# Performance work log

Measured on AMD Instinct MI355X. Metric: run time of the kernel, lower is better.

Reference implementation:

```python
import jax, jax.numpy as jnp
import numpy as np

B, N, F, H, ITERS = 128, 512, 8, 128, 3


def setup_inputs() -> dict:
    key = jax.random.key(0)
    ks = jax.random.split(key, 20)
    s = lambda d: 1.0 / np.sqrt(d)
    inp = {
        "jets": jax.random.normal(ks[0], (B, N, F), dtype=jnp.float32),
        "mask": jnp.ones((B, N), dtype=jnp.float32),
        # embedding: 2-layer MLP (emb_init=2)
        "emb_W0": jax.random.normal(ks[1], (F, H), jnp.float32) * s(F),
        "emb_b0": jnp.zeros((H,), jnp.float32),
        "emb_W1": jax.random.normal(ks[2], (H, H), jnp.float32) * s(H),
        "emb_b1": jnp.zeros((H,), jnp.float32),
        # MP layers (stacked over iters): message MLP + vertex update MLP
        "mp_Wm": jax.random.normal(ks[3], (ITERS, H, H), jnp.float32) * s(H),
        "mp_bm": jnp.zeros((ITERS, H), jnp.float32),
        "mp_Wu": jax.random.normal(ks[4], (ITERS, 2 * H, H), jnp.float32) * s(2 * H),
        "mp_bu": jnp.zeros((ITERS, H), jnp.float32),
        # simple readout: sum-pool then 2-layer MLP
        "ro_W1": jax.random.normal(ks[5], (H, H), jnp.float32) * s(H),
        "ro_b1": jnp.zeros((H,), jnp.float32),
        "ro_W2": jax.random.normal(ks[6], (H, H), jnp.float32) * s(H),
        "ro_b2": jnp.zeros((H,), jnp.float32),
    }
    return inp


def _adjacency(jets, mask):
    # fixed Gaussian-kernel affinity on raw features, row-softmax normalized
    sq = jnp.sum(jets * jets, axis=-1)                      # [B,N]
    d2 = sq[:, :, None] + sq[:, None, :] - 2.0 * jnp.einsum("bif,bjf->bij", jets, jets)
    logits = -d2 + jnp.where(mask[:, None, :] > 0, 0.0, -1e9)  # mask columns
    return jax.nn.softmax(logits, axis=-1)                  # [B,N,N]


def reference(jets, mask, emb_W0, emb_b0, emb_W1, emb_b1,
              mp_Wm, mp_bm, mp_Wu, mp_bu, ro_W1, ro_b1, ro_W2, ro_b2):
    # embedding
    h = jax.nn.relu(jnp.einsum("bnf,fh->bnh", jets, emb_W0) + emb_b0)
    h = jax.nn.relu(jnp.einsum("bnh,hk->bnk", h, emb_W1) + emb_b1)
    dij = _adjacency(jets, mask)                            # fixed across iterations
    m3 = mask[:, :, None]
    for t in range(ITERS):  # small fixed iteration count
        msg = jax.nn.relu(jnp.einsum("bnh,hk->bnk", h, mp_Wm[t]) + mp_bm[t])
        agg = jnp.einsum("bij,bjh->bih", dij, msg)          # gather+aggregate over adjacency
        h = jax.nn.relu(jnp.einsum("bnh,hk->bnk", jnp.concatenate([h, agg], axis=-1), mp_Wu[t]) + mp_bu[t])
        h = h * m3
    pooled = jnp.sum(h * m3, axis=1)                        # [B,H]
    out = jax.nn.relu(pooled @ ro_W1 + ro_b1) @ ro_W2 + ro_b2
    return out
```

## Files before the change

### kernel.cpp

```cpp
#include <hip/hip_runtime.h>
#include <stdint.h>
#include <stddef.h>

#define Bb 128
#define Nn 512
#define Hh 128
#define ROWS (Bb*Nn)

typedef __bf16 bf16;
typedef __bf16 bf16x2 __attribute__((ext_vector_type(2)));
typedef __bf16 bf16x4 __attribute__((ext_vector_type(4)));
typedef __bf16 bf16x8 __attribute__((ext_vector_type(8)));
typedef float  f32x4  __attribute__((ext_vector_type(4)));

__device__ __forceinline__ void glds16(const void* g, void* l) {
  __builtin_amdgcn_global_load_lds(
      (const __attribute__((address_space(1))) void*)g,
      (__attribute__((address_space(3))) void*)l, 16, 0, 0);
}


__global__ __launch_bounds__(256) void prep_all(
    const float* __restrict__ eW1, const float* __restrict__ Wm,
    const float* __restrict__ Wu, bf16* __restrict__ WTe,
    bf16* __restrict__ WmF, bf16* __restrict__ WuF) {
  int idx = blockIdx.x*256 + threadIdx.x;
  if (idx < 16384) {
    int k = idx >> 7, c = idx & 127;
    WTe[c*128 + (k ^ ((c & 7) << 3))] = (bf16)eW1[idx];
  } else if (idx < 65536) {
    int sub = idx - 16384;
    int s = sub >> 14, r = sub & 16383;
    int k = r >> 7, c = r & 127;
    WmF[s*16384 + (((c>>4)*4 + (k>>5))*64 + ((k>>3)&3)*16 + (c&15))*8 + (k&7)] = (bf16)Wm[sub];
  } else if (idx < 65536 + 98304) {
    int sub = idx - 65536;
    int s = sub >> 15, r = sub & 32767;
    int k = r >> 7, c = r & 127;
    WuF[s*32768 + (((c>>4)*8 + (k>>5))*64 + ((k>>3)&3)*16 + (c&15))*8 + (k&7)] = (bf16)Wu[sub];
  }
}

__global__ __launch_bounds__(256) void pmat_kernel(
    const float* __restrict__ jets, const float* __restrict__ mask,
    bf16* __restrict__ PF, float* __restrict__ rsum) {
  __shared__ float Xs[Nn*9];
  __shared__ float cbs[Nn];
  const int t = threadIdx.x;
  const int b = blockIdx.x & 127, ic = blockIdx.x >> 7;
  const int i0 = ic*128;
  const float* jb = jets + (size_t)b*Nn*8;
  for (int j = t; j < Nn; j += 256) {
    float s2 = 0.f;
#pragma unroll
    for (int f = 0; f < 8; ++f) { float v = jb[j*8+f]; Xs[j*9+f] = v; s2 = fmaf(v,v,s2); }
    cbs[j] = s2 + (mask[(size_t)b*Nn+j] > 0.f ? 0.f : 1e9f);
  }
  __syncthreads();
  const int w = t >> 6, lane = t & 63, l15 = lane & 15, g = lane >> 4;
  const int i0w = i0 + w*32;
  float xi2[2][8], sqi[2], lsum[2];
#pragma unroll
  for (int r = 0; r < 2; ++r) {
    int i = i0w + r*16 + l15;
    float sq = 0.f;
#pragma unroll
    for (int f = 0; f < 8; ++f) {
      float v = Xs[i*9+f];
      xi2[r][f] = 2.f*v;
      sq = fmaf(v, v, sq);
    }
    sqi[r] = sq;
    lsum[r] = 0.f;
  }
  bf16* Pr[2];
#pragma unroll
  for (int r = 0; r < 2; ++r) {
    int it = (i0w >> 4) + r;
    Pr[r] = PF + (((size_t)b*32 + it)*16)*512 + lane*8;
  }
#pragma unroll 2
  for (int j0 = 0; j0 < Nn; j0 += 32) {
    bf16x8 pfr[2];
#pragma unroll
    for (int e = 0; e < 8; ++e) {
      int j = j0 + 8*g + e;
      float xj[8];
#pragma unroll
      for (int f = 0; f < 8; ++f) xj[f] = Xs[j*9+f];
      float cb = cbs[j];
      float d0 = -(cb + sqi[0]);
      float d1 = -(cb + sqi[1]);
#pragma unroll
      for (int f = 0; f < 8; ++f) {
        d0 = fmaf(xi2[0][f], xj[f], d0);
        d1 = fmaf(xi2[1][f], xj[f], d1);
      }
      float ev0 = __expf(d0), ev1 = __expf(d1);
      lsum[0] += ev0; lsum[1] += ev1;
      pfr[0][e] = (bf16)ev0;
      pfr[1][e] = (bf16)ev1;
    }
#pragma unroll
    for (int r = 0; r < 2; ++r)
      *(bf16x8*)(Pr[r] + (j0 >> 5)*512) = pfr[r];
  }
#pragma unroll
  for (int r = 0; r < 2; ++r) {
    float s = lsum[r];
    s += __shfl_xor(s, 16, 64);
    s += __shfl_xor(s, 32, 64);
    if (g == 0) rsum[(size_t)b*Nn + i0w + r*16 + l15] = 1.f/s;
  }
}

__global__ __launch_bounds__(256) void embed_msg0(
    const float* __restrict__ jets, const float* __restrict__ W0,
    const float* __restrict__ b0, const bf16* __restrict__ WTe,
    const float* __restrict__ b1, const bf16* __restrict__ WmF0,
    const float* __restrict__ bm0, bf16* __restrict__ h,
    bf16* __restrict__ msgF) {
  __shared__ float sW0[8*128];
  __shared__ float sb0[128];
  __shared__ bf16 h0s[128*128];
  __shared__ bf16 sWT[128*128];
  const int t = threadIdx.x;
  const int w = t >> 6, lane = t & 63, l15 = lane & 15, g = lane >> 4;
  const int row_blk = blockIdx.x*128;
  for (int q = w; q < 32; q += 4)
    glds16((const char*)WTe + q*1024 + lane*16, (char*)(void*)sWT + q*1024);
  for (int i = t; i < 8*128; i += 256) sW0[i] = W0[i];
  if (t < 128) sb0[t] = b0[t];
  __syncthreads();
  {
    const int row = t & 127, colbase = (t >> 7) * 64;
    const float4* jp = (const float4*)(jets + ((size_t)row_blk + row)*8);
    float4 x0 = jp[0], x1 = jp[1];
    float x[8] = {x0.x,x0.y,x0.z,x0.w,x1.x,x1.y,x1.z,x1.w};
    const int sw = (row & 7) << 3;
#pragma unroll
    for (int cg = 0; cg < 16; ++cg) {
      int c0 = colbase + cg*4;
      bf16x4 o;
#pragma unroll
      for (int j = 0; j < 4; ++j) {
        float a = sb0[c0+j];
#pragma unroll
        for (int f = 0; f < 8; ++f) a = fmaf(x[f], sW0[f*128 + c0 + j], a);
        o[j] = (bf16)fmaxf(a, 0.f);
      }
      *(bf16x4*)(h0s + row*128 + (c0 ^ sw)) = o;
    }
  }
  __syncthreads();
  const int wr = (w & 1)*64, wc = (w >> 1)*64;
  f32x4 acc[4][4];
#pragma unroll
  for (int m = 0; m < 4; ++m)
#pragma unroll
    for (int n = 0; n < 4; ++n) acc[m][n] = (f32x4){0.f,0.f,0.f,0.f};
#pragma unroll
  for (int kk = 0; kk < 128; kk += 32) {
    bf16x8 bfr[4], wfr[4];
#pragma unroll
    for (int n = 0; n < 4; ++n) {
      int row = wr + n*16 + l15;
      bfr[n] = *(const bf16x8*)(h0s + row*128 + ((kk + 8*g) ^ ((row & 7) << 3)));
    }
#pragma unroll
    for (int m = 0; m < 4; ++m) {
      int c = wc + m*16 + l15;
      wfr[m] = *(const bf16x8*)(sWT + c*128 + ((kk + 8*g) ^ ((c & 7) << 3)));
    }
#pragma unroll
    for (int m = 0; m < 4; ++m)
#pragma unroll
      for (int n = 0; n < 4; ++n)
        acc[m][n] = __builtin_amdgcn_mfma_f32_16x16x32_bf16(wfr[m], bfr[n], acc[m][n], 0,0,0);
  }
  __syncthreads();
#pragma unroll
  for (int m = 0; m < 4; ++m) {
    f32x4 bs = *(const f32x4*)(b1 + wc + m*16 + g*4);
#pragma unroll
    for (int n = 0; n < 4; ++n) {
      int lr = wr + n*16 + l15;
      int r = row_blk + lr;
      int c0 = wc + m*16 + g*4;
      bf16x4 o;
#pragma unroll
      for (int j = 0; j < 4; ++j) o[j] = (bf16)fmaxf(acc[m][n][j] + bs[j], 0.f);
      *(bf16x4*)(h + (size_t)r*128 + c0) = o;
      *(bf16x4*)(h0s + lr*128 + (c0 ^ ((lr & 7) << 3))) = o;
    }
  }
  __syncthreads();
  {
    f32x4 acc2[4][4];
#pragma unroll
    for (int m = 0; m < 4; ++m)
#pragma unroll
      for (int n = 0; n < 4; ++n) acc2[m][n] = (f32x4){0.f,0.f,0.f,0.f};
#pragma unroll
    for (int kk = 0; kk < 128; kk += 32) {
      bf16x8 bfr[4], wfr[4];
#pragma unroll
      for (int n = 0; n < 4; ++n) {
        int lr = wr + n*16 + l15;
        bfr[n] = *(const bf16x8*)(h0s + lr*128 + ((kk + 8*g) ^ ((lr & 7) << 3)));
      }
#pragma unroll
      for (int m = 0; m < 4; ++m) {
        int cblk = (wc >> 4) + m;
        wfr[m] = *(const bf16x8*)(WmF0 + (size_t)(cblk*4 + (kk >> 5))*512 + lane*8);
      }
#pragma unroll
      for (int m = 0; m < 4; ++m)
#pragma unroll
        for (int n = 0; n < 4; ++n)
          acc2[m][n] = __builtin_amdgcn_mfma_f32_16x16x32_bf16(bfr[n], wfr[m], acc2[m][n], 0,0,0);
    }
    const int b = row_blk >> 9;
    const int rbase = (row_blk & 511) + wr;
#pragma unroll
    for (int m = 0; m < 4; ++m) {
      int c = wc + m*16 + l15;
      int mblk = (wc >> 4) + m;
      float bc = bm0[c];
#pragma unroll
      for (int n = 0; n < 4; ++n) {
        int rl = rbase + n*16 + g*4;
        bf16x4 o;
#pragma unroll
        for (int j = 0; j < 4; ++j) o[j] = (bf16)fmaxf(acc2[m][n][j] + bc, 0.f);
        size_t off = (size_t)b*65536 + (size_t)((rl>>5)*8 + mblk)*512
                   + (((rl>>3)&3)*16 + l15)*8 + (rl&7);
        *(bf16x4*)(msgF + off) = o;
      }
    }
  }
}

template<bool DO_MSG>
__global__ __launch_bounds__(256, 1) void iter_fused(
    const bf16* __restrict__ PF, const float* __restrict__ rsum,
    const float* __restrict__ mask, const bf16* __restrict__ msgFin,
    bf16* __restrict__ h,
    const bf16* __restrict__ WuF, const float* __restrict__ bu,
    const bf16* __restrict__ WmF, const float* __restrict__ bm,
    bf16* __restrict__ msgFout) {
  __shared__ __align__(16) char smem[65536];
  bf16* htile = (bf16*)smem;
  bf16* aggs  = (bf16*)(smem + 32768);
  const int t = threadIdx.x;
  const int b  = blockIdx.x & 127;
  const int ic = blockIdx.x >> 7;
  const int i0 = ic*128;
  const int w = t >> 6, lane = t & 63, l15 = lane & 15, g = lane >> 4;

  {
    const int i0w = i0 + w*32;
    float r_i[2];
#pragma unroll
    for (int r = 0; r < 2; ++r) r_i[r] = rsum[(size_t)b*Nn + i0w + r*16 + l15];
    f32x4 acc[2][8];
#pragma unroll
    for (int r = 0; r < 2; ++r)
#pragma unroll
      for (int m = 0; m < 8; ++m) acc[r][m] = (f32x4){0.f,0.f,0.f,0.f};
    const bf16* mBF = msgFin + (size_t)b*65536 + lane*8;
    const bf16* pBF = PF + ((size_t)b*32 + (i0w >> 4))*16*512 + lane*8;

    bf16x8 afrA[8], afrB[8], pfrA[2], pfrB[2];
    auto loadA = [&](int kt) {
#pragma unroll
      for (int m = 0; m < 8; ++m) afrA[m] = *(const bf16x8*)(mBF + (kt*8 + m)*512);
      pfrA[0] = *(const bf16x8*)(pBF + kt*512);
      pfrA[1] = *(const bf16x8*)(pBF + (16 + kt)*512);
    };
    auto loadB = [&](int kt) {
#pragma unroll
      for (int m = 0; m < 8; ++m) afrB[m] = *(const bf16x8*)(mBF + (kt*8 + m)*512);
      pfrB[0] = *(const bf16x8*)(pBF + kt*512);
      pfrB[1] = *(const bf16x8*)(pBF + (16 + kt)*512);
    };
    auto compute = [&](const bf16x8* afr, const bf16x8* pfr) {
#pragma unroll
      for (int m = 0; m < 8; ++m) {
        acc[0][m] = __builtin_amdgcn_mfma_f32_16x16x32_bf16(afr[m], pfr[0], acc[0][m], 0,0,0);
        acc[1][m] = __builtin_amdgcn_mfma_f32_16x16x32_bf16(afr[m], pfr[1], acc[1][m], 0,0,0);
      }
    };

    loadA(0);
#pragma unroll
    for (int kt = 0; kt < 16; kt += 2) {
      loadB(kt + 1);
      compute(afrA, pfrA);
      if (kt + 2 < 16) loadA(kt + 2);
      compute(afrB, pfrB);
    }
#pragma unroll
    for (int r = 0; r < 2; ++r) {
      int lr = w*32 + r*16 + l15;
#pragma unroll
      for (int m = 0; m < 8; ++m) {
        bf16x4 o;
#pragma unroll
        for (int j = 0; j < 4; ++j) o[j] = (bf16)(acc[r][m][j] * r_i[r]);
        int c0 = m*16 + g*4;
        *(bf16x4*)(aggs + lr*128 + (c0 ^ ((lr & 7) << 3))) = o;
      }
    }
  }
  __syncthreads();

  const int wr = (w & 1)*64, wc = (w >> 1)*64;
  const size_t growbase = (size_t)b*Nn + i0;
  {
    f32x4 acc[4][4];
#pragma unroll
    for (int m = 0; m < 4; ++m)
#pragma unroll
      for (int n = 0; n < 4; ++n) acc[m][n] = (f32x4){0.f,0.f,0.f,0.f};
#pragma unroll
    for (int kk = 0; kk < 256; kk += 32) {
      bf16x8 bfr[4];
      if (kk < 128) {
#pragma unroll
        for (int n = 0; n < 4; ++n)
          bfr[n] = *(const bf16x8*)(h + (growbase + wr + n*16 + l15)*128 + kk + 8*g);
      } else {
#pragma unroll
        for (int n = 0; n < 4; ++n) {
          int lr = wr + n*16 + l15;
          int kl = (kk - 128) + 8*g;
          bfr[n] = *(const bf16x8*)(aggs + lr*128 + (kl ^ ((lr & 7) << 3)));
        }
      }
      bf16x8 wfr[4];
#pragma unroll
      for (int m = 0; m < 4; ++m) {
        int cblk = (wc >> 4) + m;
        wfr[m] = *(const bf16x8*)(WuF + (size_t)(cblk*8 + (kk >> 5))*512 + lane*8);
      }
#pragma unroll
      for (int m = 0; m < 4; ++m)
#pragma unroll
        for (int n = 0; n < 4; ++n)
          acc[m][n] = __builtin_amdgcn_mfma_f32_16x16x32_bf16(wfr[m], bfr[n], acc[m][n], 0,0,0);
    }
    __syncthreads();
#pragma unroll
    for (int m = 0; m < 4; ++m) {
      f32x4 bs = *(const f32x4*)(bu + wc + m*16 + g*4);
#pragma unroll
      for (int n = 0; n < 4; ++n) {
        int lr = wr + n*16 + l15;
        size_t r = growbase + lr;
        float mv = mask[r];
        bf16x4 o;
#pragma unroll
        for (int j = 0; j < 4; ++j)
          o[j] = (bf16)(fmaxf(acc[m][n][j] + bs[j], 0.f) * mv);
        int c0 = wc + m*16 + g*4;
        *(bf16x4*)(h + r*128 + c0) = o;
        if (DO_MSG)
          *(bf16x4*)(htile + lr*128 + (c0 ^ ((lr & 7) << 3))) = o;
      }
    }
  }
  if (!DO_MSG) return;
  __syncthreads();

  {
    f32x4 acc[4][4];
#pragma unroll
    for (int m = 0; m < 4; ++m)
#pragma unroll
      for (int n = 0; n < 4; ++n) acc[m][n] = (f32x4){0.f,0.f,0.f,0.f};
#pragma unroll
    for (int kk = 0; kk < 128; kk += 32) {
      bf16x8 bfr[4], wfr[4];
#pragma unroll
      for (int n = 0; n < 4; ++n) {
        int lr = wr + n*16 + l15;
        bfr[n] = *(const bf16x8*)(htile + lr*128 + ((kk + 8*g) ^ ((lr & 7) << 3)));
      }
#pragma unroll
      for (int m = 0; m < 4; ++m) {
        int cblk = (wc >> 4) + m;
        wfr[m] = *(const bf16x8*)(WmF + (size_t)(cblk*4 + (kk >> 5))*512 + lane*8);
      }
#pragma unroll
      for (int m = 0; m < 4; ++m)
#pragma unroll
        for (int n = 0; n < 4; ++n)
          acc[m][n] = __builtin_amdgcn_mfma_f32_16x16x32_bf16(bfr[n], wfr[m], acc[m][n], 0,0,0);
    }
#pragma unroll
    for (int m = 0; m < 4; ++m) {
      int c = wc + m*16 + l15;
      int mblk = (wc >> 4) + m;
      float bc = bm[c];
#pragma unroll
      for (int n = 0; n < 4; ++n) {
        int rl = i0 + wr + n*16 + g*4;
        bf16x4 o;
#pragma unroll
        for (int j = 0; j < 4; ++j) o[j] = (bf16)fmaxf(acc[m][n][j] + bc, 0.f);
        size_t off = (size_t)b*65536 + (size_t)((rl>>5)*8 + mblk)*512
                   + (((rl>>3)&3)*16 + l15)*8 + (rl&7);
        *(bf16x4*)(msgFout + off) = o;
      }
    }
  }
}

__global__ __launch_bounds__(256) void pool_readout(
    const bf16* __restrict__ h, const float* __restrict__ mask,
    const float* __restrict__ W1, const float* __restrict__ b1,
    const float* __restrict__ W2, const float* __restrict__ b2,
    float* __restrict__ out) {
  __shared__ float part[3][128];
  __shared__ float pl[128];
  __shared__ float hid[128];
  int b = blockIdx.x, t = threadIdx.x, g = t >> 6, cp = (t & 63)*2;
  float a0 = 0.f, a1 = 0.f;
  for (int n = g*128; n < g*128+128; ++n) {
    float mv = mask[(size_t)b*Nn + n];
    bf16x2 v = *(const bf16x2*)(h + ((size_t)b*Nn + n)*128 + cp);
    a0 = fmaf((float)v[0], mv, a0);
    a1 = fmaf((float)v[1], mv, a1);
  }
  if (g > 0) { part[g-1][cp] = a0; part[g-1][cp+1] = a1; }
  __syncthreads();
  if (g == 0) {
    pl[cp]   = a0 + part[0][cp]   + part[1][cp]   + part[2][cp];
    pl[cp+1] = a1 + part[0][cp+1] + part[1][cp+1] + part[2][cp+1];
  }
  __syncthreads();
  if (t < 128) {
    float a = b1[t];
#pragma unroll 4
    for (int j = 0; j < 128; ++j) a = fmaf(pl[j], W1[j*128 + t], a);
    hid[t] = fmaxf(a, 0.f);
  }
  __syncthreads();
  if (t < 128) {
    float a = b2[t];
#pragma unroll 4
    for (int j = 0; j < 128; ++j) a = fmaf(hid[j], W2[j*128 + t], a);
    out[(size_t)b*128 + t] = a;
  }
}

extern "C" void kernel_launch(void* const* d_in, const int* in_sizes, int n_in,
                              void* d_out, int out_size, void* d_ws, size_t ws_size,
                              hipStream_t stream) {
  const float* jets = (const float*)d_in[0];
  const float* mask = (const float*)d_in[1];
  const float* eW0  = (const float*)d_in[2];
  const float* eb0  = (const float*)d_in[3];
  const float* eW1  = (const float*)d_in[4];
  const float* eb1  = (const float*)d_in[5];
  const float* Wm   = (const float*)d_in[6];
  const float* bm   = (const float*)d_in[7];
  const float* Wu   = (const float*)d_in[8];
  const float* bu   = (const float*)d_in[9];
  const float* rW1  = (const float*)d_in[10];
  const float* rb1  = (const float*)d_in[11];
  const float* rW2  = (const float*)d_in[12];
  const float* rb2  = (const float*)d_in[13];
  float* out = (float*)d_out;

  bf16* h     = (bf16*)d_ws;
  bf16* msgFA = h     + (size_t)ROWS*128;
  bf16* msgFB = msgFA + (size_t)ROWS*128;
  bf16* PF    = msgFB + (size_t)ROWS*128;
  bf16* WTe   = PF    + (size_t)Bb*512*512;
  bf16* WmF   = WTe   + 128*128;
  bf16* WuF   = WmF   + 3*128*128;
  float* rsum = (float*)(WuF + 3*256*128);

  prep_all<<<640, 256, 0, stream>>>(eW1, Wm, Wu, WTe, WmF, WuF);
  pmat_kernel<<<Bb*4, 256, 0, stream>>>(jets, mask, PF, rsum);
  embed_msg0<<<ROWS/128, 256, 0, stream>>>(jets, eW0, eb0, WTe, eb1,
                                           WmF, bm, h, msgFA);
  iter_fused<true><<<Bb*4, 256, 0, stream>>>(
      PF, rsum, mask, msgFA, h,
      WuF, bu, WmF + (size_t)1*128*128, bm + 1*128, msgFB);
  iter_fused<true><<<Bb*4, 256, 0, stream>>>(
      PF, rsum, mask, msgFB, h,
      WuF + (size_t)1*256*128, bu + 1*128,
      WmF + (size_t)2*128*128, bm + 2*128, msgFA);
  iter_fused<false><<<Bb*4, 256, 0, stream>>>(
      PF, rsum, mask, msgFA, h,
      WuF + (size_t)2*256*128, bu + 2*128, nullptr, nullptr, nullptr);

  pool_readout<<<Bb, 256, 0, stream>>>(h, mask, rW1, rb1, rW2, rb2, out);
}
```

Before: 158.5 us.

## Fuse adjacency matrix generation into first message-passing iteration kernel

Result: slower. 167.9 us (+5.9%).

```diff
diff --git a/kernel.cpp b/kernel.cpp
--- a/kernel.cpp
+++ b/kernel.cpp
@@ -41,79 +41,6 @@
   }
 }
 
-__global__ __launch_bounds__(256) void pmat_kernel(
-    const float* __restrict__ jets, const float* __restrict__ mask,
-    bf16* __restrict__ PF, float* __restrict__ rsum) {
-  __shared__ float Xs[Nn*9];
-  __shared__ float cbs[Nn];
-  const int t = threadIdx.x;
-  const int b = blockIdx.x & 127, ic = blockIdx.x >> 7;
-  const int i0 = ic*128;
-  const float* jb = jets + (size_t)b*Nn*8;
-  for (int j = t; j < Nn; j += 256) {
-    float s2 = 0.f;
-#pragma unroll
-    for (int f = 0; f < 8; ++f) { float v = jb[j*8+f]; Xs[j*9+f] = v; s2 = fmaf(v,v,s2); }
-    cbs[j] = s2 + (mask[(size_t)b*Nn+j] > 0.f ? 0.f : 1e9f);
-  }
-  __syncthreads();
-  const int w = t >> 6, lane = t & 63, l15 = lane & 15, g = lane >> 4;
-  const int i0w = i0 + w*32;
-  float xi2[2][8], sqi[2], lsum[2];
-#pragma unroll
-  for (int r = 0; r < 2; ++r) {
-    int i = i0w + r*16 + l15;
-    float sq = 0.f;
-#pragma unroll
-    for (int f = 0; f < 8; ++f) {
-      float v = Xs[i*9+f];
-      xi2[r][f] = 2.f*v;
-      sq = fmaf(v, v, sq);
-    }
-    sqi[r] = sq;
-    lsum[r] = 0.f;
-  }
-  bf16* Pr[2];
-#pragma unroll
-  for (int r = 0; r < 2; ++r) {
-    int it = (i0w >> 4) + r;
-    Pr[r] = PF + (((size_t)b*32 + it)*16)*512 + lane*8;
-  }
-#pragma unroll 2
-  for (int j0 = 0; j0 < Nn; j0 += 32) {
-    bf16x8 pfr[2];
-#pragma unroll
-    for (int e = 0; e < 8; ++e) {
-      int j = j0 + 8*g + e;
-      float xj[8];
-#pragma unroll
-      for (int f = 0; f < 8; ++f) xj[f] = Xs[j*9+f];
-      float cb = cbs[j];
-      float d0 = -(cb + sqi[0]);
-      float d1 = -(cb + sqi[1]);
-#pragma unroll
-      for (int f = 0; f < 8; ++f) {
-        d0 = fmaf(xi2[0][f], xj[f], d0);
-        d1 = fmaf(xi2[1][f], xj[f], d1);
-      }
-      float ev0 = __expf(d0), ev1 = __expf(d1);
-      lsum[0] += ev0; lsum[1] += ev1;
-      pfr[0][e] = (bf16)ev0;
-      pfr[1][e] = (bf16)ev1;
-    }
-#pragma unroll
-    for (int r = 0; r < 2; ++r)
-      *(bf16x8*)(Pr[r] + (j0 >> 5)*512) = pfr[r];
-  }
-#pragma unroll
-  for (int r = 0; r < 2; ++r) {
-    float s = lsum[r];
-    s += __shfl_xor(s, 16, 64);
-    s += __shfl_xor(s, 32, 64);
-    if (g == 0) rsum[(size_t)b*Nn + i0w + r*16 + l15] = 1.f/s;
-  }
-}
-
 __global__ __launch_bounds__(256) void embed_msg0(
     const float* __restrict__ jets, const float* __restrict__ W0,
     const float* __restrict__ b0, const bf16* __restrict__ WTe,
@@ -241,9 +168,10 @@
   }
 }
 
-template<bool DO_MSG>
+template<bool COMPUTE_P, bool DO_MSG>
 __global__ __launch_bounds__(256, 1) void iter_fused(
-    const bf16* __restrict__ PF, const float* __restrict__ rsum,
+    const float* __restrict__ jets, bf16* __restrict__ PF,
+    float* __restrict__ rsum,
     const float* __restrict__ mask, const bf16* __restrict__ msgFin,
     bf16* __restrict__ h,
     const bf16* __restrict__ WuF, const float* __restrict__ bu,
@@ -252,38 +180,95 @@
   __shared__ __align__(16) char smem[65536];
   bf16* htile = (bf16*)smem;
   bf16* aggs  = (bf16*)(smem + 32768);
+  float* Xs   = (float*)smem;
+  float* cbs  = (float*)(smem + 18432);
   const int t = threadIdx.x;
   const int b  = blockIdx.x & 127;
   const int ic = blockIdx.x >> 7;
   const int i0 = ic*128;
   const int w = t >> 6, lane = t & 63, l15 = lane & 15, g = lane >> 4;
 
+  if (COMPUTE_P) {
+    const float* jb = jets + (size_t)b*Nn*8;
+    for (int j = t; j < Nn; j += 256) {
+      float s2 = 0.f;
+#pragma unroll
+      for (int f = 0; f < 8; ++f) { float v = jb[j*8+f]; Xs[j*9+f] = v; s2 = fmaf(v,v,s2); }
+      cbs[j] = s2 + (mask[(size_t)b*Nn+j] > 0.f ? 0.f : 1e9f);
+    }
+    __syncthreads();
+  }
+
   {
     const int i0w = i0 + w*32;
-    float r_i[2];
-#pragma unroll
-    for (int r = 0; r < 2; ++r) r_i[r] = rsum[(size_t)b*Nn + i0w + r*16 + l15];
+    float r_i[2], lsum[2] = {0.f, 0.f};
+    float xi2[2][8], sqi[2];
+    if (COMPUTE_P) {
+#pragma unroll
+      for (int r = 0; r < 2; ++r) {
+        int i = i0w + r*16 + l15;
+        float sq = 0.f;
+#pragma unroll
+        for (int f = 0; f < 8; ++f) {
+          float v = Xs[i*9+f];
+          xi2[r][f] = 2.f*v;
+          sq = fmaf(v, v, sq);
+        }
+        sqi[r] = sq;
+      }
+    } else {
+#pragma unroll
+      for (int r = 0; r < 2; ++r) r_i[r] = rsum[(size_t)b*Nn + i0w + r*16 + l15];
+    }
     f32x4 acc[2][8];
 #pragma unroll
     for (int r = 0; r < 2; ++r)
 #pragma unroll
       for (int m = 0; m < 8; ++m) acc[r][m] = (f32x4){0.f,0.f,0.f,0.f};
     const bf16* mBF = msgFin + (size_t)b*65536 + lane*8;
-    const bf16* pBF = PF + ((size_t)b*32 + (i0w >> 4))*16*512 + lane*8;
+    bf16* pBF = PF + ((size_t)b*32 + (i0w >> 4))*16*512 + lane*8;
 
     bf16x8 afrA[8], afrB[8], pfrA[2], pfrB[2];
-    auto loadA = [&](int kt) {
+    auto loadAfrA = [&](int kt) {
 #pragma unroll
       for (int m = 0; m < 8; ++m) afrA[m] = *(const bf16x8*)(mBF + (kt*8 + m)*512);
+    };
+    auto loadAfrB = [&](int kt) {
+#pragma unroll
+      for (int m = 0; m < 8; ++m) afrB[m] = *(const bf16x8*)(mBF + (kt*8 + m)*512);
+    };
+    auto loadPfrA = [&](int kt) {
       pfrA[0] = *(const bf16x8*)(pBF + kt*512);
       pfrA[1] = *(const bf16x8*)(pBF + (16 + kt)*512);
     };
-    auto loadB = [&](int kt) {
-#pragma unroll
-      for (int m = 0; m < 8; ++m) afrB[m] = *(const bf16x8*)(mBF + (kt*8 + m)*512);
+    auto loadPfrB = [&](int kt) {
       pfrB[0] = *(const bf16x8*)(pBF + kt*512);
       pfrB[1] = *(const bf16x8*)(pBF + (16 + kt)*512);
     };
+    auto makeP = [&](int kt, bf16x8* pfr) {
+      int j0 = kt*32;
+#pragma unroll
+      for (int e = 0; e < 8; ++e) {
+        int j = j0 + 8*g + e;
+        float xj[8];
+#pragma unroll
+        for (int f = 0; f < 8; ++f) xj[f] = Xs[j*9+f];
+        float cb = cbs[j];
+        float d0 = -(cb + sqi[0]);
+        float d1 = -(cb + sqi[1]);
+#pragma unroll
+        for (int f = 0; f < 8; ++f) {
+          d0 = fmaf(xi2[0][f], xj[f], d0);
+          d1 = fmaf(xi2[1][f], xj[f], d1);
+        }
+        float ev0 = __expf(d0), ev1 = __expf(d1);
+        lsum[0] += ev0; lsum[1] += ev1;
+        pfr[0][e] = (bf16)ev0;
+        pfr[1][e] = (bf16)ev1;
+      }
+      *(bf16x8*)(pBF + kt*512)        = pfr[0];
+      *(bf16x8*)(pBF + (16 + kt)*512) = pfr[1];
+    };
     auto compute = [&](const bf16x8* afr, const bf16x8* pfr) {
 #pragma unroll
       for (int m = 0; m < 8; ++m) {
@@ -292,13 +277,27 @@
       }
     };
 
-    loadA(0);
+    loadAfrA(0);
+    if (!COMPUTE_P) loadPfrA(0);
 #pragma unroll
     for (int kt = 0; kt < 16; kt += 2) {
-      loadB(kt + 1);
+      loadAfrB(kt + 1);
+      if (COMPUTE_P) makeP(kt, pfrA); else loadPfrB(kt + 1);
       compute(afrA, pfrA);
-      if (kt + 2 < 16) loadA(kt + 2);
+      if (kt + 2 < 16) loadAfrA(kt + 2);
+      if (COMPUTE_P) makeP(kt + 1, pfrB);
+      else if (kt + 2 < 16) loadPfrA(kt + 2);
       compute(afrB, pfrB);
+    }
+    if (COMPUTE_P) {
+#pragma unroll
+      for (int r = 0; r < 2; ++r) {
+        float s = lsum[r];
+        s += __shfl_xor(s, 16, 64);
+        s += __shfl_xor(s, 32, 64);
+        r_i[r] = 1.f/s;
+        if (g == 0) rsum[(size_t)b*Nn + i0w + r*16 + l15] = r_i[r];
+      }
     }
 #pragma unroll
     for (int r = 0; r < 2; ++r) {
@@ -484,18 +483,17 @@
   float* rsum = (float*)(WuF + 3*256*128);
 
   prep_all<<<640, 256, 0, stream>>>(eW1, Wm, Wu, WTe, WmF, WuF);
-  pmat_kernel<<<Bb*4, 256, 0, stream>>>(jets, mask, PF, rsum);
   embed_msg0<<<ROWS/128, 256, 0, stream>>>(jets, eW0, eb0, WTe, eb1,
                                            WmF, bm, h, msgFA);
-  iter_fused<true><<<Bb*4, 256, 0, stream>>>(
-      PF, rsum, mask, msgFA, h,
+  iter_fused<true,true><<<Bb*4, 256, 0, stream>>>(
+      jets, PF, rsum, mask, msgFA, h,
       WuF, bu, WmF + (size_t)1*128*128, bm + 1*128, msgFB);
-  iter_fused<true><<<Bb*4, 256, 0, stream>>>(
-      PF, rsum, mask, msgFB, h,
+  iter_fused<false,true><<<Bb*4, 256, 0, stream>>>(
+      jets, PF, rsum, mask, msgFB, h,
       WuF + (size_t)1*256*128, bu + 1*128,
       WmF + (size_t)2*128*128, bm + 2*128, msgFA);
-  iter_fused<false><<<Bb*4, 256, 0, stream>>>(
-      PF, rsum, mask, msgFA, h,
+  iter_fused<false,false><<<Bb*4, 256, 0, stream>>>(
+      jets, PF, rsum, mask, msgFA, h,
       WuF + (size_t)2*256*128, bu + 2*128, nullptr, nullptr, nullptr);
 
   pool_readout<<<Bb, 256, 0, stream>>>(h, mask, rW1, rb1, rW2, rb2, out);
```
